# Optimization experiments

Measured on AMD Instinct MI355X. Metric: run time of the kernel, lower is better.

## Reference

```python
import jax, jax.numpy as jnp
import numpy as np

N_NODES = 100000
N_EDGES = 600000
N_GRAPHS = 2000
HIDDEN = 128
LAYERS = 6
VOCAB = 128


def setup_inputs() -> dict:
    key = jax.random.key(0)
    ks = jax.random.split(key, 8)
    scale = 1.0 / np.sqrt(HIDDEN)  # keep activations stable across 6 layers
    x_tokens = jax.random.randint(ks[0], (N_NODES,), 0, VOCAB, dtype=jnp.int32)
    edge_index = jax.random.randint(ks[1], (2, N_EDGES), 0, N_NODES, dtype=jnp.int32)
    batch = jnp.sort(jax.random.randint(ks[2], (N_NODES,), 0, N_GRAPHS, dtype=jnp.int32))
    emb = jax.random.normal(ks[3], (VOCAB, HIDDEN), dtype=jnp.float32)
    W1 = jax.random.normal(ks[4], (LAYERS, HIDDEN, HIDDEN), dtype=jnp.float32) * scale
    b1 = jnp.zeros((LAYERS, HIDDEN), dtype=jnp.float32)
    W2 = jax.random.normal(ks[5], (LAYERS, HIDDEN, HIDDEN), dtype=jnp.float32) * scale
    b2 = jnp.zeros((LAYERS, HIDDEN), dtype=jnp.float32)
    return {"x_tokens": x_tokens, "edge_index": edge_index, "batch": batch,
            "emb": emb, "W1": W1, "b1": b1, "W2": W2, "b2": b2}


def reference(x_tokens, edge_index, batch, emb, W1, b1, W2, b2):
    src, dst = edge_index[0], edge_index[1]
    # AtomEncoder: embedding lookup
    x = emb[x_tokens]  # [N, H]
    # GIN layers: out = MLP((1+eps)*x + sum_{j->i} x_j), eps=0 (GINConv default)
    for l in range(LAYERS):
        agg = jax.ops.segment_sum(x[src], dst, num_segments=N_NODES)  # scatter-add
        h = x + agg
        h = jax.nn.relu(h @ W1[l] + b1[l])
        h = h @ W2[l] + b2[l]
        x = jax.nn.relu(h)  # dropout is identity at inference
    # global mean pool over per-graph node sets
    sums = jax.ops.segment_sum(x, batch, num_segments=N_GRAPHS)
    counts = jax.ops.segment_sum(jnp.ones((N_NODES,), x.dtype), batch, num_segments=N_GRAPHS)
    g = sums / jnp.maximum(counts, 1.0)[:, None]
    return g
```

## Files before the change

### kernel.cpp

```cpp
#include <hip/hip_runtime.h>

#define HD  128
#define TM  32
#define SYB 136

typedef __attribute__((ext_vector_type(8))) short    short8;
typedef __attribute__((ext_vector_type(8))) _Float16 half8;
typedef __attribute__((ext_vector_type(4))) float    float4v;

__device__ __forceinline__ void split_bf(float v, short& hi, short& lo) {
    unsigned bv = __float_as_uint(v);
    unsigned hb = (bv + 0x7FFFu + ((bv >> 16) & 1u)) & 0xFFFF0000u;
    hi = (short)(hb >> 16);
    float r = v - __uint_as_float(hb);
    unsigned rv = __float_as_uint(r);
    lo = (short)((rv + 0x7FFFu + ((rv >> 16) & 1u)) >> 16);
}

__global__ void k_embed(const int* __restrict__ tok, const float* __restrict__ emb,
                        _Float16* __restrict__ x, int n)
{
    int g = blockIdx.x * 256 + threadIdx.x;
    if (g < n * 16) {
        int node = g >> 4, part = g & 15;
        const float4* e4 = (const float4*)emb + ((size_t)tok[node] << 5) + part * 2;
        float4 a = e4[0], b = e4[1];
        half8 h;
        h[0] = (_Float16)a.x; h[1] = (_Float16)a.y; h[2] = (_Float16)a.z; h[3] = (_Float16)a.w;
        h[4] = (_Float16)b.x; h[5] = (_Float16)b.y; h[6] = (_Float16)b.z; h[7] = (_Float16)b.w;
        ((half8*)x)[g] = h;
    }
}

__global__ void k_degree(const int* __restrict__ dst, int* __restrict__ deg, int e)
{
    int i = blockIdx.x * 256 + threadIdx.x;
    if (i < e) atomicAdd(&deg[dst[i]], 1);
}

__global__ void k_scan1(const int* __restrict__ deg, int* __restrict__ rp,
                        int* __restrict__ bsum, int n)
{
    __shared__ int s[1024];
    int t = threadIdx.x;
    int i = blockIdx.x * 1024 + t;
    int v = (i < n) ? deg[i] : 0;
    s[t] = v; __syncthreads();
    for (int off = 1; off < 1024; off <<= 1) {
        int tmp = (t >= off) ? s[t - off] : 0;
        __syncthreads();
        s[t] += tmp;
        __syncthreads();
    }
    if (i < n) rp[i] = s[t] - v;
    if (t == 1023) bsum[blockIdx.x] = s[1023];
}

__global__ void k_scan2(int* __restrict__ bsum, int nb)
{
    __shared__ int s[128];
    int t = threadIdx.x;
    int v = (t < nb) ? bsum[t] : 0;
    s[t] = v; __syncthreads();
    for (int off = 1; off < 128; off <<= 1) {
        int tmp = (t >= off) ? s[t - off] : 0;
        __syncthreads();
        s[t] += tmp;
        __syncthreads();
    }
    if (t < nb) bsum[t] = s[t] - v;
}

__global__ void k_scan3(int* __restrict__ rp, const int* __restrict__ bsum, int n, int e)
{
    int i = blockIdx.x * 1024 + threadIdx.x;
    if (i < n) rp[i] += bsum[blockIdx.x];
    if (i == 0) rp[n] = e;
}

__global__ void k_fill(const int* __restrict__ src, const int* __restrict__ dst,
                       const int* __restrict__ rp, int* __restrict__ fill,
                       int* __restrict__ ci, int e)
{
    int i = blockIdx.x * 256 + threadIdx.x;
    if (i < e) {
        int d = dst[i];
        int p = atomicAdd(&fill[d], 1);
        ci[rp[d] + p] = src[i];
    }
}

__global__ void k_wsplit(const float* __restrict__ W1, const float* __restrict__ W2,
                         short* __restrict__ wh, short* __restrict__ wl, int total)
{
    int g = blockIdx.x * 256 + threadIdx.x;
    if (g >= total) return;
    int f  = g & 16383;
    int m  = (g >> 14) & 1;
    int l  = g >> 15;
    int j    = f & 7;
    int lane = (f >> 3) & 63;
    int kb   = (f >> 9) & 3;
    int ct   = f >> 11;
    int k  = kb * 32 + (lane >> 4) * 8 + j;
    int nn = ct * 16 + (lane & 15);
    const float* W = m ? W2 : W1;
    float v = W[(size_t)l * 16384 + k * 128 + nn];
    short h, lo; split_bf(v, h, lo);
    wh[g] = h; wl[g] = lo;
}

__global__ __launch_bounds__(256, 4)
void k_gin(const _Float16* __restrict__ xin, _Float16* __restrict__ xout,
           const int* __restrict__ rp, const int* __restrict__ ci,
           const short* __restrict__ w1h, const short* __restrict__ w1l,
           const short* __restrict__ w2h, const short* __restrict__ w2l,
           const float* __restrict__ b1, const float* __restrict__ b2,
           int n)
{
    __shared__ short sAh[TM * SYB];
    __shared__ short sAl[TM * SYB];

    const int tx   = threadIdx.x;
    const int row0 = blockIdx.x * TM;
    const int wv   = tx >> 6, lane = tx & 63;
    const int quad = lane >> 4, lrow = lane & 15;

    {
        const int rl = tx >> 3, part = tx & 7;
        int node = row0 + rl;
        if (node >= n) node = n - 1;
        const half8* xr = (const half8*)(xin + (size_t)node * HD);
        half8 xs0 = xr[part * 2 + 0];
        half8 xs1 = xr[part * 2 + 1];
        float acc[2][8];
#pragma unroll
        for (int k = 0; k < 8; ++k) { acc[0][k] = (float)xs0[k]; acc[1][k] = (float)xs1[k]; }

        const int e0 = rp[node], e1 = rp[node + 1];
        for (int eb = e0; eb < e1; eb += 8) {
            int idx = eb + part;
            int c = (idx < e1) ? ci[idx] : node;
#pragma unroll
            for (int j = 0; j < 8; ++j) {
                int cj = __shfl(c, j, 8);
                const half8* xc = (const half8*)(xin + (size_t)cj * HD);
                half8 v0 = xc[part * 2 + 0];
                half8 v1 = xc[part * 2 + 1];
#pragma unroll
                for (int k = 0; k < 8; ++k) {
                    acc[0][k] += (float)v0[k];
                    acc[1][k] += (float)v1[k];
                }
            }
        }
        int deg = e1 - e0;
        if (deg) {
            float fx = (float)(((deg + 7) & ~7) - deg);
#pragma unroll
            for (int k = 0; k < 8; ++k) {
                acc[0][k] -= fx * (float)xs0[k];
                acc[1][k] -= fx * (float)xs1[k];
            }
        }
#pragma unroll
        for (int q = 0; q < 2; ++q) {
            short8 h8s, l8s;
#pragma unroll
            for (int k = 0; k < 8; ++k) { short h, l; split_bf(acc[q][k], h, l); h8s[k] = h; l8s[k] = l; }
            int off = rl * SYB + part * 16 + q * 8;
            *(short8*)&sAh[off] = h8s;
            *(short8*)&sAl[off] = l8s;
        }
    }

    short8 Bh[2][4];
    {
        const short8* h8 = (const short8*)w1h;
#pragma unroll
        for (int c = 0; c < 2; ++c)
#pragma unroll
            for (int kb = 0; kb < 4; ++kb)
                Bh[c][kb] = h8[((2 * wv + c) * 4 + kb) * 64 + lane];
    }
    float bb0 = b1[(2 * wv + 0) * 16 + lrow];
    float bb1 = b1[(2 * wv + 1) * 16 + lrow];
    __syncthreads();

    float4v acc1[2][2];
#pragma unroll
    for (int rt = 0; rt < 2; ++rt) {
        acc1[rt][0] = (float4v){bb0, bb0, bb0, bb0};
        acc1[rt][1] = (float4v){bb1, bb1, bb1, bb1};
    }
    {
        const short8* l8 = (const short8*)w1l;
#pragma unroll
        for (int kb = 0; kb < 4; ++kb) {
            short8 Ah[2], Al[2];
#pragma unroll
            for (int rt = 0; rt < 2; ++rt) {
                int off = (rt * 16 + lrow) * SYB + kb * 32 + quad * 8;
                Ah[rt] = *(const short8*)&sAh[off];
                Al[rt] = *(const short8*)&sAl[off];
            }
            short8 Bl0 = l8[((2 * wv + 0) * 4 + kb) * 64 + lane];
            short8 Bl1 = l8[((2 * wv + 1) * 4 + kb) * 64 + lane];
#pragma unroll
            for (int rt = 0; rt < 2; ++rt) {
                acc1[rt][0] = __builtin_amdgcn_mfma_f32_16x16x32_bf16(Ah[rt], Bh[0][kb], acc1[rt][0], 0, 0, 0);
                acc1[rt][0] = __builtin_amdgcn_mfma_f32_16x16x32_bf16(Al[rt], Bh[0][kb], acc1[rt][0], 0, 0, 0);
                acc1[rt][0] = __builtin_amdgcn_mfma_f32_16x16x32_bf16(Ah[rt], Bl0,       acc1[rt][0], 0, 0, 0);
                acc1[rt][1] = __builtin_amdgcn_mfma_f32_16x16x32_bf16(Ah[rt], Bh[1][kb], acc1[rt][1], 0, 0, 0);
                acc1[rt][1] = __builtin_amdgcn_mfma_f32_16x16x32_bf16(Al[rt], Bh[1][kb], acc1[rt][1], 0, 0, 0);
                acc1[rt][1] = __builtin_amdgcn_mfma_f32_16x16x32_bf16(Ah[rt], Bl1,       acc1[rt][1], 0, 0, 0);
            }
        }
    }

    short8 Bh2[2][4];
    {
        const short8* h8 = (const short8*)w2h;
#pragma unroll
        for (int c = 0; c < 2; ++c)
#pragma unroll
            for (int kb = 0; kb < 4; ++kb)
                Bh2[c][kb] = h8[((2 * wv + c) * 4 + kb) * 64 + lane];
    }
    float cb0 = b2[(2 * wv + 0) * 16 + lrow];
    float cb1 = b2[(2 * wv + 1) * 16 + lrow];

    __syncthreads();

#pragma unroll
    for (int rt = 0; rt < 2; ++rt)
#pragma unroll
        for (int c = 0; c < 2; ++c) {
            int col = (2 * wv + c) * 16 + lrow;
#pragma unroll
            for (int r = 0; r < 4; ++r) {
                int row = rt * 16 + quad * 4 + r;
                float v = fmaxf(acc1[rt][c][r], 0.f);
                short h, l; split_bf(v, h, l);
                sAh[row * SYB + col] = h;
                sAl[row * SYB + col] = l;
            }
        }
    __syncthreads();

    float4v acc2[2][2];
#pragma unroll
    for (int rt = 0; rt < 2; ++rt) {
        acc2[rt][0] = (float4v){cb0, cb0, cb0, cb0};
        acc2[rt][1] = (float4v){cb1, cb1, cb1, cb1};
    }
    {
        const short8* l8 = (const short8*)w2l;
#pragma unroll
        for (int kb = 0; kb < 4; ++kb) {
            short8 Ah[2], Al[2];
#pragma unroll
            for (int rt = 0; rt < 2; ++rt) {
                int off = (rt * 16 + lrow) * SYB + kb * 32 + quad * 8;
                Ah[rt] = *(const short8*)&sAh[off];
                Al[rt] = *(const short8*)&sAl[off];
            }
            short8 Bl0 = l8[((2 * wv + 0) * 4 + kb) * 64 + lane];
            short8 Bl1 = l8[((2 * wv + 1) * 4 + kb) * 64 + lane];
#pragma unroll
            for (int rt = 0; rt < 2; ++rt) {
                acc2[rt][0] = __builtin_amdgcn_mfma_f32_16x16x32_bf16(Ah[rt], Bh2[0][kb], acc2[rt][0], 0, 0, 0);
                acc2[rt][0] = __builtin_amdgcn_mfma_f32_16x16x32_bf16(Al[rt], Bh2[0][kb], acc2[rt][0], 0, 0, 0);
                acc2[rt][0] = __builtin_amdgcn_mfma_f32_16x16x32_bf16(Ah[rt], Bl0,        acc2[rt][0], 0, 0, 0);
                acc2[rt][1] = __builtin_amdgcn_mfma_f32_16x16x32_bf16(Ah[rt], Bh2[1][kb], acc2[rt][1], 0, 0, 0);
                acc2[rt][1] = __builtin_amdgcn_mfma_f32_16x16x32_bf16(Al[rt], Bh2[1][kb], acc2[rt][1], 0, 0, 0);
                acc2[rt][1] = __builtin_amdgcn_mfma_f32_16x16x32_bf16(Ah[rt], Bl1,        acc2[rt][1], 0, 0, 0);
            }
        }
    }

#pragma unroll
    for (int rt = 0; rt < 2; ++rt)
#pragma unroll
        for (int c = 0; c < 2; ++c) {
            int col = (2 * wv + c) * 16 + lrow;
#pragma unroll
            for (int r = 0; r < 4; ++r) {
                int node = row0 + rt * 16 + quad * 4 + r;
                if (node < n)
                    xout[(size_t)node * HD + col] = (_Float16)fmaxf(acc2[rt][c][r], 0.f);
            }
        }
}

__global__ void k_pool(const _Float16* __restrict__ x, const int* __restrict__ batch,
                       float* __restrict__ out, int n)
{
    int g = blockIdx.x, t = threadIdx.x;
    int lo = 0, hi = n;
    while (lo < hi) { int m = (lo + hi) >> 1; if (batch[m] < g) lo = m + 1; else hi = m; }
    int s = lo;
    hi = n;
    while (lo < hi) { int m = (lo + hi) >> 1; if (batch[m] < g + 1) lo = m + 1; else hi = m; }
    int e = lo;
    float sum = 0.f;
    for (int i = s; i < e; ++i) sum += (float)x[(size_t)i * HD + t];
    int cnt = e - s;
    out[(size_t)g * HD + t] = (cnt > 0) ? sum / (float)cnt : 0.f;
}

extern "C" void kernel_launch(void* const* d_in, const int* in_sizes, int n_in,
                              void* d_out, int out_size, void* d_ws, size_t ws_size,
                              hipStream_t stream)
{
    const int*   tok   = (const int*)d_in[0];
    const int*   eidx  = (const int*)d_in[1];
    const int*   batch = (const int*)d_in[2];
    const float* emb   = (const float*)d_in[3];
    const float* W1    = (const float*)d_in[4];
    const float* b1    = (const float*)d_in[5];
    const float* W2    = (const float*)d_in[6];
    const float* b2    = (const float*)d_in[7];
    float* out = (float*)d_out;

    const int n      = in_sizes[0];
    const int e      = in_sizes[1] / 2;
    const int ngraph = out_size / HD;
    const int L      = in_sizes[4] / (HD * HD);
    const int* src = eidx;
    const int* dst = eidx + e;

    char* w = (char*)d_ws;
    size_t off = 0;
    auto alloc = [&](size_t bytes) -> void* {
        void* p = w + off;
        off = (off + bytes + 255) & ~(size_t)255;
        return p;
    };
    _Float16* xa = (_Float16*)alloc((size_t)(n + TM) * HD * 2);
    _Float16* xb = (_Float16*)alloc((size_t)(n + TM) * HD * 2);
    int* rp    = (int*)alloc((size_t)(n + 1) * 4);
    size_t zoff = off;
    int* deg   = (int*)alloc((size_t)n * 4);
    int* fillc = (int*)alloc((size_t)n * 4);
    size_t zbytes = off - zoff;
    int* ci    = (int*)alloc((size_t)e * 4);
    int* bsum  = (int*)alloc(512);
    short* wh  = (short*)alloc((size_t)L * 2 * 16384 * 2);
    short* wl  = (short*)alloc((size_t)L * 2 * 16384 * 2);

    hipMemsetAsync(deg, 0, zbytes, stream);

    k_embed<<<(n * 16 + 255) / 256, 256, 0, stream>>>(tok, emb, xa, n);

    int wtot = L * 2 * 16384;
    k_wsplit<<<(wtot + 255) / 256, 256, 0, stream>>>(W1, W2, wh, wl, wtot);

    k_degree<<<(e + 255) / 256, 256, 0, stream>>>(dst, deg, e);
    int nb = (n + 1023) / 1024;
    k_scan1<<<nb, 1024, 0, stream>>>(deg, rp, bsum, n);
    k_scan2<<<1, 128, 0, stream>>>(bsum, nb);
    k_scan3<<<nb, 1024, 0, stream>>>(rp, bsum, n, e);
    k_fill<<<(e + 255) / 256, 256, 0, stream>>>(src, dst, rp, fillc, ci, e);

    _Float16* xin = xa;
    _Float16* xo  = xb;
    for (int l = 0; l < L; ++l) {
        const short* lw = wh + (size_t)l * 2 * 16384;
        const short* ll = wl + (size_t)l * 2 * 16384;
        k_gin<<<(n + TM - 1) / TM, 256, 0, stream>>>(
            xin, xo, rp, ci,
            lw, ll, lw + 16384, ll + 16384,
            b1 + (size_t)l * HD, b2 + (size_t)l * HD, n);
        _Float16* t = xin; xin = xo; xo = t;
    }

    k_pool<<<ngraph, HD, 0, stream>>>(xin, batch, out, n);
}
```

Before: 437.0 us.

## Fuse preprocessing kernels and stage tile edge lists in shared memory

Merges the embedding, weight-split and degree-count kernels into one launch that dispatches on block index, removing two launches. In the GIN kernel, each block cooperatively loads its tile's contiguous CSR column indices into shared memory, then walks exact per-node edge ranges two at a time. This replaces the shuffle-based padded loop and its correction for padded self-reads. The occupancy hint rises from 4 to 6 blocks per CU, which may force register spills, and the extra __syncthreads per chunk adds barrier cost.

```diff
diff --git a/kernel.cpp b/kernel.cpp
--- a/kernel.cpp
+++ b/kernel.cpp
@@ -1,8 +1,9 @@
 #include <hip/hip_runtime.h>
 
-#define HD  128
-#define TM  32
-#define SYB 136
+#define HD   128
+#define TM   32
+#define SYB  136
+#define ECAP 512
 
 typedef __attribute__((ext_vector_type(8))) short    short8;
 typedef __attribute__((ext_vector_type(8))) _Float16 half8;
@@ -17,25 +18,46 @@
     lo = (short)((rv + 0x7FFFu + ((rv >> 16) & 1u)) >> 16);
 }
 
-__global__ void k_embed(const int* __restrict__ tok, const float* __restrict__ emb,
-                        _Float16* __restrict__ x, int n)
-{
-    int g = blockIdx.x * 256 + threadIdx.x;
-    if (g < n * 16) {
-        int node = g >> 4, part = g & 15;
-        const float4* e4 = (const float4*)emb + ((size_t)tok[node] << 5) + part * 2;
-        float4 a = e4[0], b = e4[1];
-        half8 h;
-        h[0] = (_Float16)a.x; h[1] = (_Float16)a.y; h[2] = (_Float16)a.z; h[3] = (_Float16)a.w;
-        h[4] = (_Float16)b.x; h[5] = (_Float16)b.y; h[6] = (_Float16)b.z; h[7] = (_Float16)b.w;
-        ((half8*)x)[g] = h;
-    }
-}
-
-__global__ void k_degree(const int* __restrict__ dst, int* __restrict__ deg, int e)
-{
-    int i = blockIdx.x * 256 + threadIdx.x;
-    if (i < e) atomicAdd(&deg[dst[i]], 1);
+__global__ void k_pre(const int* __restrict__ tok, const float* __restrict__ emb,
+                      _Float16* __restrict__ x, int n,
+                      const float* __restrict__ W1, const float* __restrict__ W2,
+                      short* __restrict__ wh, short* __restrict__ wl, int wtot,
+                      const int* __restrict__ dst, int* __restrict__ deg, int e,
+                      int nbE, int nbW)
+{
+    int b = blockIdx.x, tx = threadIdx.x;
+    if (b < nbE) {
+        int g = b * 256 + tx;
+        if (g < n * 16) {
+            int node = g >> 4, part = g & 15;
+            const float4* e4 = (const float4*)emb + ((size_t)tok[node] << 5) + part * 2;
+            float4 a = e4[0], c = e4[1];
+            half8 h;
+            h[0] = (_Float16)a.x; h[1] = (_Float16)a.y; h[2] = (_Float16)a.z; h[3] = (_Float16)a.w;
+            h[4] = (_Float16)c.x; h[5] = (_Float16)c.y; h[6] = (_Float16)c.z; h[7] = (_Float16)c.w;
+            ((half8*)x)[g] = h;
+        }
+    } else if (b < nbE + nbW) {
+        int g = (b - nbE) * 256 + tx;
+        if (g < wtot) {
+            int f  = g & 16383;
+            int m  = (g >> 14) & 1;
+            int l  = g >> 15;
+            int j    = f & 7;
+            int lane = (f >> 3) & 63;
+            int kb   = (f >> 9) & 3;
+            int ct   = f >> 11;
+            int k  = kb * 32 + (lane >> 4) * 8 + j;
+            int nn = ct * 16 + (lane & 15);
+            const float* W = m ? W2 : W1;
+            float v = W[(size_t)l * 16384 + k * 128 + nn];
+            short h, lo; split_bf(v, h, lo);
+            wh[g] = h; wl[g] = lo;
+        }
+    } else {
+        int i = (b - nbE - nbW) * 256 + tx;
+        if (i < e) atomicAdd(&deg[dst[i]], 1);
+    }
 }
 
 __global__ void k_scan1(const int* __restrict__ deg, int* __restrict__ rp,
@@ -90,27 +112,7 @@
     }
 }
 
-__global__ void k_wsplit(const float* __restrict__ W1, const float* __restrict__ W2,
-                         short* __restrict__ wh, short* __restrict__ wl, int total)
-{
-    int g = blockIdx.x * 256 + threadIdx.x;
-    if (g >= total) return;
-    int f  = g & 16383;
-    int m  = (g >> 14) & 1;
-    int l  = g >> 15;
-    int j    = f & 7;
-    int lane = (f >> 3) & 63;
-    int kb   = (f >> 9) & 3;
-    int ct   = f >> 11;
-    int k  = kb * 32 + (lane >> 4) * 8 + j;
-    int nn = ct * 16 + (lane & 15);
-    const float* W = m ? W2 : W1;
-    float v = W[(size_t)l * 16384 + k * 128 + nn];
-    short h, lo; split_bf(v, h, lo);
-    wh[g] = h; wl[g] = lo;
-}
-
-__global__ __launch_bounds__(256, 4)
+__global__ __launch_bounds__(256, 6)
 void k_gin(const _Float16* __restrict__ xin, _Float16* __restrict__ xout,
            const int* __restrict__ rp, const int* __restrict__ ci,
            const short* __restrict__ w1h, const short* __restrict__ w1l,
@@ -120,6 +122,7 @@
 {
     __shared__ short sAh[TM * SYB];
     __shared__ short sAl[TM * SYB];
+    __shared__ int   sCI[ECAP];
 
     const int tx   = threadIdx.x;
     const int row0 = blockIdx.x * TM;
@@ -138,31 +141,45 @@
         for (int k = 0; k < 8; ++k) { acc[0][k] = (float)xs0[k]; acc[1][k] = (float)xs1[k]; }
 
         const int e0 = rp[node], e1 = rp[node + 1];
-        for (int eb = e0; eb < e1; eb += 8) {
-            int idx = eb + part;
-            int c = (idx < e1) ? ci[idx] : node;
-#pragma unroll
-            for (int j = 0; j < 8; ++j) {
-                int cj = __shfl(c, j, 8);
-                const half8* xc = (const half8*)(xin + (size_t)cj * HD);
-                half8 v0 = xc[part * 2 + 0];
-                half8 v1 = xc[part * 2 + 1];
+        const int eb0 = rp[row0];
+        const int ebN = rp[(row0 + TM < n) ? (row0 + TM) : n];
+
+        for (int t0 = eb0; t0 < ebN; t0 += ECAP) {
+            const int t1 = (t0 + ECAP < ebN) ? (t0 + ECAP) : ebN;
+            for (int i = tx; i < t1 - t0; i += 256) sCI[i] = ci[t0 + i];
+            __syncthreads();
+
+            int a = (e0 > t0) ? e0 : t0;
+            int b = (e1 < t1) ? e1 : t1;
+            int ee = a;
+            for (; ee + 1 < b; ee += 2) {
+                int c0 = sCI[ee - t0];
+                int c1 = sCI[ee + 1 - t0];
+                const half8* xc0 = (const half8*)(xin + (size_t)c0 * HD);
+                const half8* xc1 = (const half8*)(xin + (size_t)c1 * HD);
+                half8 u0 = xc0[part * 2 + 0], u1 = xc0[part * 2 + 1];
+                half8 v0 = xc1[part * 2 + 0], v1 = xc1[part * 2 + 1];
 #pragma unroll
                 for (int k = 0; k < 8; ++k) {
-                    acc[0][k] += (float)v0[k];
-                    acc[1][k] += (float)v1[k];
+                    acc[0][k] = fmaf((float)u0[k], 1.0f, acc[0][k]);
+                    acc[1][k] = fmaf((float)u1[k], 1.0f, acc[1][k]);
+                    acc[0][k] = fmaf((float)v0[k], 1.0f, acc[0][k]);
+                    acc[1][k] = fmaf((float)v1[k], 1.0f, acc[1][k]);
                 }
             }
-        }
-        int deg = e1 - e0;
-        if (deg) {
-            float fx = (float)(((deg + 7) & ~7) - deg);
-#pragma unroll
-            for (int k = 0; k < 8; ++k) {
-                acc[0][k] -= fx * (float)xs0[k];
-                acc[1][k] -= fx * (float)xs1[k];
-            }
-        }
+            if (ee < b) {
+                int c0 = sCI[ee - t0];
+                const half8* xc0 = (const half8*)(xin + (size_t)c0 * HD);
+                half8 u0 = xc0[part * 2 + 0], u1 = xc0[part * 2 + 1];
+#pragma unroll
+                for (int k = 0; k < 8; ++k) {
+                    acc[0][k] = fmaf((float)u0[k], 1.0f, acc[0][k]);
+                    acc[1][k] = fmaf((float)u1[k], 1.0f, acc[1][k]);
+                }
+            }
+            __syncthreads();
+        }
+
 #pragma unroll
         for (int q = 0; q < 2; ++q) {
             short8 h8s, l8s;
@@ -351,12 +368,14 @@
 
     hipMemsetAsync(deg, 0, zbytes, stream);
 
-    k_embed<<<(n * 16 + 255) / 256, 256, 0, stream>>>(tok, emb, xa, n);
-
     int wtot = L * 2 * 16384;
-    k_wsplit<<<(wtot + 255) / 256, 256, 0, stream>>>(W1, W2, wh, wl, wtot);
-
-    k_degree<<<(e + 255) / 256, 256, 0, stream>>>(dst, deg, e);
+    int nbE = (n * 16 + 255) / 256;
+    int nbW = (wtot + 255) / 256;
+    int nbD = (e + 255) / 256;
+    k_pre<<<nbE + nbW + nbD, 256, 0, stream>>>(tok, emb, xa, n,
+                                               W1, W2, wh, wl, wtot,
+                                               dst, deg, e, nbE, nbW);
+
     int nb = (n + 1023) / 1024;
     k_scan1<<<nb, 1024, 0, stream>>>(deg, rp, bsum, n);
     k_scan2<<<1, 128, 0, stream>>>(bsum, nb);
```

Result: no change. 429.7 us (-1.7%).
